# Optimization experiments

Hardware: AMD Instinct MI355X
Metric: run time of the kernel (lower is better)

## Reference

```python
import jax, jax.numpy as jnp
import numpy as np

# Static hyperparams matching init_kwargs
KSIZE, STRIDE, PAD, DIL = 3, 2, 1, 1


def setup_inputs() -> dict:
    key = jax.random.key(0)
    k1, k2 = jax.random.split(key)
    B, H, W, Cin, Cout = 8, 128, 128, 128, 256
    feats = jax.random.normal(k1, (B * H * W, Cin), dtype=jnp.float32)
    weight = jax.random.normal(k2, (KSIZE * KSIZE, Cin, Cout), dtype=jnp.float32) * 0.05
    alpha_upper = jnp.ones((1,), dtype=jnp.float32)
    # dense grid coords [N, 3] = (batch, y, x), matching a dense image sparse tensor
    bb, yy, xx = np.meshgrid(np.arange(B), np.arange(H), np.arange(W), indexing='ij')
    coords = jnp.asarray(np.stack([bb, yy, xx], -1).reshape(-1, 3), dtype=jnp.int32)
    return {"feats": feats, "weight": weight, "alpha_upper": alpha_upper,
            "coords": coords, "H": H, "W": W, "B": B}


def _coord_ranges(H, W):
    # Faithful translation of WrappedMinkowskiStridedOperation.__init__ + forward
    # coordinate math, specialized to a dense grid (per-batch min=0, max=H-1/W-1).
    kernel_origin = DIL * ((KSIZE - 1) // 2) * (KSIZE % 2)
    dilated = DIL * (KSIZE - 1) + 1
    ks_off = kernel_origin - dilated + 1          # _kernel_start_offset
    ke_off = kernel_origin                        # _kernel_end_offset
    idx_start = kernel_origin - PAD               # _index_start_offset
    ranges = []
    for ext in (H, W):
        idx_end = (ext - 1) + kernel_origin + PAD - dilated + 2
        start = max(idx_start, (0 + ks_off - idx_start) // STRIDE * STRIDE + idx_start)
        end = min(idx_end, ((ext - 1 + ke_off - idx_start) // STRIDE + 1) * STRIDE + idx_start)
        ranges.append(np.arange(start, end, STRIDE))
    offsets = np.arange(KSIZE) * DIL - kernel_origin  # kernel region offsets
    return ranges[0], ranges[1], offsets, idx_start


def reference(feats, weight, alpha_upper, coords, H, W, B):
    Cin = feats.shape[1]
    Cout = weight.shape[-1]
    ys, xs, offs, idx_start = _coord_ranges(H, W)
    OH, OW = len(ys), len(xs)
    oy, ox = jnp.meshgrid(jnp.asarray(ys, jnp.int32), jnp.asarray(xs, jnp.int32), indexing='ij')
    dy, dx = np.meshgrid(offs, offs, indexing='ij')
    dy = jnp.asarray(dy.reshape(-1), jnp.int32)  # [kvol]
    dx = jnp.asarray(dx.reshape(-1), jnp.int32)
    ny = oy[None] + dy[:, None, None]            # [kvol, OH, OW]
    nx = ox[None] + dx[:, None, None]
    valid = (ny >= 0) & (ny < H) & (nx >= 0) & (nx < W)
    lin = jnp.clip(ny, 0, H - 1) * W + jnp.clip(nx, 0, W - 1)  # [kvol, OH, OW]
    feats3 = feats.reshape(B, H * W, Cin)
    gathered = feats3[:, lin]                    # [B, kvol, OH, OW, Cin]
    gathered = jnp.where(valid[None, ..., None], gathered, jnp.zeros((), feats.dtype))
    out = jnp.einsum('bkhwc,kcd->bhwd', gathered, weight)  # [B, OH, OW, Cout]
    out_feats = out.reshape(B * OH * OW, Cout)
    # output coordinates, remapped as in forward (shift by index_start, divide by stride)
    oc = jnp.stack([oy, ox], -1).reshape(-1, 2)  # [OH*OW, 2]
    oc = (oc - jnp.int32(idx_start)) // jnp.int32(STRIDE)
    oc = jnp.tile(oc, (B, 1))
    bcol = jnp.repeat(jnp.arange(B, dtype=jnp.int32), OH * OW)
    out_coords = jnp.concatenate([bcol[:, None], oc], axis=1)
    return out_feats, out_coords, alpha_upper
```

## Files before the change

kernel.cpp:

```cpp
#include <hip/hip_runtime.h>


#define OUT_FEATS_ELEMS (32768 * 256)
#define OUT_COORDS_OFF  OUT_FEATS_ELEMS
#define ALPHA_OFF       (OUT_FEATS_ELEMS + 32768 * 3)

typedef float v16f __attribute__((ext_vector_type(16)));

__device__ __forceinline__ unsigned pk4fp8(float a, float b, float c, float d) {
    unsigned u = 0;
    u = __builtin_amdgcn_cvt_pk_fp8_f32(a, b, u, false);
    u = __builtin_amdgcn_cvt_pk_fp8_f32(c, d, u, true);
    return u;
}

#define GLOAD_LDS16(SRC, DST)                                                  \
    __builtin_amdgcn_global_load_lds(                                          \
        (const __attribute__((address_space(1))) void*)(SRC),                  \
        (__attribute__((address_space(3))) void*)(DST), 16, 0, 0)

__global__ void prep_kernel(const float* __restrict__ feats, const float* __restrict__ w,
                            const float* __restrict__ alpha,
                            unsigned char* __restrict__ F8, unsigned char* __restrict__ Bw,
                            float* __restrict__ out) {
    int bid = blockIdx.x;
    if (bid < 8192) {
        int i = bid * 256 + threadIdx.x;
        const float4* f = (const float4*)feats;
        float4 a = f[2 * i];
        float4 b = f[2 * i + 1];
        uint2 r;
        r.x = pk4fp8(a.x, a.y, a.z, a.w);
        r.y = pk4fp8(b.x, b.y, b.z, b.w);
        ((uint2*)F8)[i] = r;
        return;
    }
    int cid = (bid - 8192) * 256 + threadIdx.x;
    if (cid < 32768) {
        int b = cid >> 12, iy = (cid >> 6) & 63, ix = cid & 63;
        float* c = out + OUT_COORDS_OFF + (size_t)cid * 3;
        c[0] = (float)b; c[1] = (float)iy; c[2] = (float)ix;
        if (cid == 0) out[ALPHA_OFF] = alpha[0];
    }
    if (cid < 18432) {
        int ch  = cid & 7;
        int row = (cid >> 3) & 127;
        int t   = cid >> 10;
        int nb  = (t >= 9) ? 1 : 0;
        int tap = t - 9 * nb;
        int chp = ch ^ (row & 7);
        int n   = (nb << 7) + row;
        int kb  = (tap << 7) + (chp << 4);
        unsigned u[4];
#pragma unroll
        for (int q = 0; q < 4; ++q) {
            float f0 = w[(size_t)(kb + 4 * q + 0) * 256 + n];
            float f1 = w[(size_t)(kb + 4 * q + 1) * 256 + n];
            float f2 = w[(size_t)(kb + 4 * q + 2) * 256 + n];
            float f3 = w[(size_t)(kb + 4 * q + 3) * 256 + n];
            u[q] = pk4fp8(f0, f1, f2, f3);
        }
        uint4 r; r.x = u[0]; r.y = u[1]; r.z = u[2]; r.w = u[3];
        *(uint4*)(Bw + (size_t)cid * 16) = r;
    }
}

__global__ void coords_alpha_kernel(float* __restrict__ out, const float* __restrict__ alpha) {
    int i = blockIdx.x * 256 + threadIdx.x;
    int b = i >> 12, iy = (i >> 6) & 63, ix = i & 63;
    float* c = out + OUT_COORDS_OFF + (size_t)i * 3;
    c[0] = (float)b; c[1] = (float)iy; c[2] = (float)ix;
    if (i == 0) out[ALPHA_OFF] = alpha[0];
}

__global__ __launch_bounds__(256, 2) void gemm_conv_kernel(
    const unsigned char* __restrict__ F8,
    const unsigned char* __restrict__ Bw,
    float* __restrict__ out)
{
    __shared__ unsigned char At[2][128 * 128];
    __shared__ unsigned char Bs[2][128 * 128];

    const int tid  = threadIdx.x;
    const int bid  = blockIdx.x;
    const int nb   = bid >> 8;
    const int my   = ((bid & 7) << 5) + ((bid >> 3) & 31);
    const int n0   = nb << 7;
    const int m0   = my << 7;
    const int bb   = my >> 5;
    const int iy0  = (my << 1) & 63;

    const int lane = tid & 63, wave = tid >> 6;
    const int wm   = (wave >> 1) << 6;
    const int wn   = (wave & 1) << 6;
    const int l31  = lane & 31;
    const int hh   = lane >> 5;
    const int xorl = l31 & 7;

    const int srow = lane >> 3;
    const int chp  = (lane & 7) ^ srow;
    const long rowA0 = (long)bb << 14;
    const unsigned char* bimg = Bw + ((size_t)(nb * 9) << 14) + ((size_t)wave << 12) + ((size_t)lane << 4);

    v16f acc[2][2];
#pragma unroll
    for (int i = 0; i < 2; i++)
#pragma unroll
        for (int j = 0; j < 2; j++) acc[i][j] = (v16f)(0.0f);

    auto stage = [&](int tap, int b) {
        const int dy = tap / 3 - 1;
        const int dx = tap % 3 - 1;
        unsigned char* adst0 = At[b] + (wave << 12);
        unsigned char* bdst0 = Bs[b] + (wave << 12);
#pragma unroll
        for (int it = 0; it < 4; ++it) {
            const int region = (wave << 2) + it;
            GLOAD_LDS16(bimg + ((size_t)tap << 14) + (it << 10), bdst0 + (it << 10));
            const int row = (region << 3) + srow;
            const int iyl = row >> 6, ix = row & 63;
            const int ny  = ((iy0 + iyl) << 1) + dy;
            const int nx  = (ix << 1) + dx;
            if (((unsigned)ny < 128u) & ((unsigned)nx < 128u)) {
                const unsigned char* asrc =
                    F8 + ((rowA0 + ((long)ny << 7) + nx) << 7) + (chp << 4);
                GLOAD_LDS16(asrc, adst0 + (it << 10));
            } else {
                uint4 z; z.x = 0u; z.y = 0u; z.z = 0u; z.w = 0u;
                *(uint4*)(At[b] + (region << 10) + (lane << 4)) = z;
            }
        }
    };

    stage(0, 0);

    for (int tap = 0; tap < 9; ++tap) {
        const int b = tap & 1;
        __syncthreads();
        if (tap < 8) stage(tap + 1, b ^ 1);

#pragma unroll
        for (int seg = 0; seg < 8; ++seg) {
            const int q = seg ^ xorl;
            long long a[2], bb2[2];
#pragma unroll
            for (int i = 0; i < 2; i++)
                a[i] = *(const long long*)(At[b] + ((wm + (i << 5) + l31) << 7) + (q << 4) + (hh << 3));
#pragma unroll
            for (int j = 0; j < 2; j++)
                bb2[j] = *(const long long*)(Bs[b] + ((wn + (j << 5) + l31) << 7) + (q << 4) + (hh << 3));
#pragma unroll
            for (int i = 0; i < 2; i++)
#pragma unroll
                for (int j = 0; j < 2; j++)
                    acc[i][j] = __builtin_amdgcn_mfma_f32_32x32x16_fp8_fp8(a[i], bb2[j], acc[i][j], 0, 0, 0);
        }
    }

#pragma unroll
    for (int i = 0; i < 2; i++)
#pragma unroll
        for (int j = 0; j < 2; j++) {
            const int gcol = n0 + wn + (j << 5) + l31;
#pragma unroll
            for (int r = 0; r < 16; ++r) {
                const int grow = m0 + wm + (i << 5) + (r & 3) + ((r >> 2) << 3) + (hh << 2);
                __builtin_nontemporal_store(acc[i][j][r], &out[(size_t)grow * 256 + gcol]);
            }
        }
}

__global__ void naive_conv_kernel(const float* __restrict__ feats,
                                  const float* __restrict__ w,
                                  float* __restrict__ out) {
    int m = blockIdx.x;
    int n = threadIdx.x;
    int bb = m >> 12, iy = (m >> 6) & 63, ix = m & 63;
    float acc = 0.f;
    for (int tap = 0; tap < 9; ++tap) {
        int ny = 2 * iy + tap / 3 - 1;
        int nx = 2 * ix + tap % 3 - 1;
        if ((unsigned)ny < 128u && (unsigned)nx < 128u) {
            const float* fr = feats + ((size_t)((bb << 14) + (ny << 7) + nx) << 7);
            const float* wr = w + tap * 32768 + n;
            for (int c = 0; c < 128; ++c) acc += fr[c] * wr[c * 256];
        }
    }
    out[(size_t)m * 256 + n] = acc;
}

extern "C" void kernel_launch(void* const* d_in, const int* in_sizes, int n_in,
                              void* d_out, int out_size, void* d_ws, size_t ws_size,
                              hipStream_t stream) {
    const float* feats  = (const float*)d_in[0];
    const float* weight = (const float*)d_in[1];
    const float* alpha  = (const float*)d_in[2];
    float* out = (float*)d_out;

    const size_t NEED = (size_t)16777216 + (size_t)18 * 16384;
    if (ws_size >= NEED) {
        unsigned char* F8 = (unsigned char*)d_ws;
        unsigned char* Bw = F8 + 16777216;
        prep_kernel<<<8336, 256, 0, stream>>>(feats, weight, alpha, F8, Bw, out);
        gemm_conv_kernel<<<512, 256, 0, stream>>>(F8, Bw, out);
    } else {
        coords_alpha_kernel<<<128, 256, 0, stream>>>(out, alpha);
        naive_conv_kernel<<<32768, 256, 0, stream>>>(feats, weight, out);
    }
}
```

Baseline: 134.4 us.

## Widen GEMM block to full 256 N with triple-buffered LDS pipeline

The conv GEMM kernel now uses 512-thread blocks that each compute a 128x256 output tile. Each gathered A tile is therefore loaded once for all output channels instead of once per N half. Staging moves from double to triple buffering with explicit vmcnt waits and barriers, so two taps are in flight ahead of compute. Out-of-bounds rows load from a zeroed scratch page instead of taking a branch that writes zeros to LDS, and MFMA sections run at raised wave priority. The cost is about 144KB of LDS per block, leaving one block per CU and half as many blocks overall, which may reduce latency hiding.

```diff
diff --git a/kernel.cpp b/kernel.cpp
--- a/kernel.cpp
+++ b/kernel.cpp
@@ -4,6 +4,10 @@
 #define OUT_FEATS_ELEMS (32768 * 256)
 #define OUT_COORDS_OFF  OUT_FEATS_ELEMS
 #define ALPHA_OFF       (OUT_FEATS_ELEMS + 32768 * 3)
+
+#define F8_BYTES   16777216
+#define BW_BYTES   (18 * 16384)
+#define ZP_OFF     (F8_BYTES + BW_BYTES)
 
 typedef float v16f __attribute__((ext_vector_type(16)));
 
@@ -42,6 +46,10 @@
         c[0] = (float)b; c[1] = (float)iy; c[2] = (float)ix;
         if (cid == 0) out[ALPHA_OFF] = alpha[0];
     }
+    if (cid < 8) {
+        uint4 z; z.x = 0u; z.y = 0u; z.z = 0u; z.w = 0u;
+        *(uint4*)(Bw + BW_BYTES + cid * 16) = z;
+    }
     if (cid < 18432) {
         int ch  = cid & 7;
         int row = (cid >> 3) & 127;
@@ -73,26 +81,24 @@
     if (i == 0) out[ALPHA_OFF] = alpha[0];
 }
 
-__global__ __launch_bounds__(256, 2) void gemm_conv_kernel(
+__global__ __launch_bounds__(512, 2) void gemm_conv_kernel(
     const unsigned char* __restrict__ F8,
     const unsigned char* __restrict__ Bw,
     float* __restrict__ out)
 {
-    __shared__ unsigned char At[2][128 * 128];
-    __shared__ unsigned char Bs[2][128 * 128];
+    __shared__ unsigned char At[3][128 * 128];
+    __shared__ unsigned char Bs[3][256 * 128];
 
     const int tid  = threadIdx.x;
     const int bid  = blockIdx.x;
-    const int nb   = bid >> 8;
-    const int my   = ((bid & 7) << 5) + ((bid >> 3) & 31);
-    const int n0   = nb << 7;
+    const int my   = ((bid & 7) << 5) + (bid >> 3);
     const int m0   = my << 7;
     const int bb   = my >> 5;
     const int iy0  = (my << 1) & 63;
 
     const int lane = tid & 63, wave = tid >> 6;
-    const int wm   = (wave >> 1) << 6;
-    const int wn   = (wave & 1) << 6;
+    const int wm   = (wave >> 2) << 6;
+    const int wn   = (wave & 3) << 6;
     const int l31  = lane & 31;
     const int hh   = lane >> 5;
     const int xorl = l31 & 7;
@@ -100,7 +106,9 @@
     const int srow = lane >> 3;
     const int chp  = (lane & 7) ^ srow;
     const long rowA0 = (long)bb << 14;
-    const unsigned char* bimg = Bw + ((size_t)(nb * 9) << 14) + ((size_t)wave << 12) + ((size_t)lane << 4);
+    const unsigned char* zp = Bw + BW_BYTES;
+    const unsigned char* bsrc0 = Bw + ((size_t)((wave >> 2) * 9) << 14)
+                                    + ((size_t)(wave & 3) << 12) + ((size_t)lane << 4);
 
     v16f acc[2][2];
 #pragma unroll
@@ -108,60 +116,74 @@
 #pragma unroll
         for (int j = 0; j < 2; j++) acc[i][j] = (v16f)(0.0f);
 
-    auto stage = [&](int tap, int b) {
+    auto stage = [&](int tap, int buf) {
         const int dy = tap / 3 - 1;
         const int dx = tap % 3 - 1;
-        unsigned char* adst0 = At[b] + (wave << 12);
-        unsigned char* bdst0 = Bs[b] + (wave << 12);
-#pragma unroll
-        for (int it = 0; it < 4; ++it) {
-            const int region = (wave << 2) + it;
-            GLOAD_LDS16(bimg + ((size_t)tap << 14) + (it << 10), bdst0 + (it << 10));
+        const unsigned char* bs = bsrc0 + ((size_t)tap << 14);
+        unsigned char* bdst = Bs[buf] + (wave << 12);
+#pragma unroll
+        for (int q = 0; q < 4; ++q)
+            GLOAD_LDS16(bs + (q << 10), bdst + (q << 10));
+        unsigned char* adst = At[buf] + (wave << 11);
+#pragma unroll
+        for (int it = 0; it < 2; ++it) {
+            const int region = (wave << 1) + it;
             const int row = (region << 3) + srow;
-            const int iyl = row >> 6, ix = row & 63;
+            const int iyl = region >> 3;
             const int ny  = ((iy0 + iyl) << 1) + dy;
-            const int nx  = (ix << 1) + dx;
-            if (((unsigned)ny < 128u) & ((unsigned)nx < 128u)) {
-                const unsigned char* asrc =
-                    F8 + ((rowA0 + ((long)ny << 7) + nx) << 7) + (chp << 4);
-                GLOAD_LDS16(asrc, adst0 + (it << 10));
-            } else {
-                uint4 z; z.x = 0u; z.y = 0u; z.z = 0u; z.w = 0u;
-                *(uint4*)(At[b] + (region << 10) + (lane << 4)) = z;
-            }
+            const int nx  = ((row & 63) << 1) + dx;
+            const unsigned char* asrc =
+                (((unsigned)ny < 128u) & ((unsigned)nx < 128u))
+                    ? F8 + ((rowA0 + ((long)ny << 7) + nx) << 7) + (chp << 4)
+                    : zp + (chp << 4);
+            GLOAD_LDS16(asrc, adst + (it << 10));
         }
     };
 
-    stage(0, 0);
-
-    for (int tap = 0; tap < 9; ++tap) {
-        const int b = tap & 1;
-        __syncthreads();
-        if (tap < 8) stage(tap + 1, b ^ 1);
-
+    auto compute = [&](int buf) {
 #pragma unroll
         for (int seg = 0; seg < 8; ++seg) {
             const int q = seg ^ xorl;
-            long long a[2], bb2[2];
+            long long a[2], b2[2];
 #pragma unroll
             for (int i = 0; i < 2; i++)
-                a[i] = *(const long long*)(At[b] + ((wm + (i << 5) + l31) << 7) + (q << 4) + (hh << 3));
+                a[i] = *(const long long*)(At[buf] + ((wm + (i << 5) + l31) << 7) + (q << 4) + (hh << 3));
 #pragma unroll
             for (int j = 0; j < 2; j++)
-                bb2[j] = *(const long long*)(Bs[b] + ((wn + (j << 5) + l31) << 7) + (q << 4) + (hh << 3));
+                b2[j] = *(const long long*)(Bs[buf] + ((wn + (j << 5) + l31) << 7) + (q << 4) + (hh << 3));
+            __builtin_amdgcn_s_setprio(1);
 #pragma unroll
             for (int i = 0; i < 2; i++)
 #pragma unroll
                 for (int j = 0; j < 2; j++)
-                    acc[i][j] = __builtin_amdgcn_mfma_f32_32x32x16_fp8_fp8(a[i], bb2[j], acc[i][j], 0, 0, 0);
-        }
+                    acc[i][j] = __builtin_amdgcn_mfma_f32_32x32x16_fp8_fp8(a[i], b2[j], acc[i][j], 0, 0, 0);
+            __builtin_amdgcn_s_setprio(0);
+        }
+    };
+
+    stage(0, 0);
+    stage(1, 1);
+
+#pragma unroll
+    for (int tap = 0; tap < 9; ++tap) {
+        const int buf = tap % 3;
+        if (tap < 7) {
+            stage(tap + 2, (tap + 2) % 3);
+            asm volatile("s_waitcnt vmcnt(12)\ns_barrier" ::: "memory");
+        } else if (tap == 7) {
+            asm volatile("s_waitcnt vmcnt(6)\ns_barrier" ::: "memory");
+        } else {
+            asm volatile("s_waitcnt vmcnt(0)\ns_barrier" ::: "memory");
+        }
+        compute(tap == 8 ? 2 : buf);
+        asm volatile("s_barrier" ::: "memory");
     }
 
 #pragma unroll
     for (int i = 0; i < 2; i++)
 #pragma unroll
         for (int j = 0; j < 2; j++) {
-            const int gcol = n0 + wn + (j << 5) + l31;
+            const int gcol = wn + (j << 5) + l31;
 #pragma unroll
             for (int r = 0; r < 16; ++r) {
                 const int grow = m0 + wm + (i << 5) + (r & 3) + ((r >> 2) << 3) + (hh << 2);
@@ -197,12 +219,12 @@
     const float* alpha  = (const float*)d_in[2];
     float* out = (float*)d_out;
 
-    const size_t NEED = (size_t)16777216 + (size_t)18 * 16384;
+    const size_t NEED = (size_t)F8_BYTES + BW_BYTES + 128;
     if (ws_size >= NEED) {
         unsigned char* F8 = (unsigned char*)d_ws;
-        unsigned char* Bw = F8 + 16777216;
+        unsigned char* Bw = F8 + F8_BYTES;
         prep_kernel<<<8336, 256, 0, stream>>>(feats, weight, alpha, F8, Bw, out);
-        gemm_conv_kernel<<<512, 256, 0, stream>>>(F8, Bw, out);
+        gemm_conv_kernel<<<256, 512, 0, stream>>>(F8, Bw, out);
     } else {
         coords_alpha_kernel<<<128, 256, 0, stream>>>(out, alpha);
         naive_conv_kernel<<<32768, 256, 0, stream>>>(feats, weight, out);
```

New measurement: 135.9 us. About the same (+1.1%).
